# Kernel optimization log

Measured on AMD Instinct MI355X. Metric: run time of the kernel, lower is better.

Reference implementation:

```python
import jax, jax.numpy as jnp
import numpy as np
from jax import lax

B, L, D_MODEL = 2, 1024, 768
N_LAYER, D_STATE, D_CONV, EXPAND = 8, 16, 4, 2
D_INNER = EXPAND * D_MODEL          # 1536
DT_RANK = -(-D_MODEL // 16)         # 48 (MambaConfig 'auto')


def setup_inputs() -> dict:
    key = jax.random.key(0)
    ks = jax.random.split(key, 10)
    s = 0.02
    batch = jax.random.normal(ks[0], (B, D_MODEL, L), jnp.float32)
    lengths = jax.random.randint(ks[1], (B,), L // 2, L + 1)
    mask = jnp.arange(L)[None, :] < lengths[:, None]          # valid-prefix mask [B,L]
    norm_w = jnp.ones((N_LAYER, D_MODEL), jnp.float32)
    W_in = jax.random.normal(ks[2], (N_LAYER, 2 * D_INNER, D_MODEL), jnp.float32) * s
    conv_w = jax.random.normal(ks[3], (N_LAYER, D_INNER, D_CONV), jnp.float32) * 0.5
    conv_b = jnp.zeros((N_LAYER, D_INNER), jnp.float32)
    W_x = jax.random.normal(ks[4], (N_LAYER, DT_RANK + 2 * D_STATE, D_INNER), jnp.float32) * s
    W_dt = jax.random.normal(ks[5], (N_LAYER, D_INNER, DT_RANK), jnp.float32) * (DT_RANK ** -0.5)
    # mamba dt init: dt ~ logU[1e-3, 0.1], bias = softplus^-1(dt)
    dt = jnp.exp(jax.random.uniform(ks[6], (N_LAYER, D_INNER)) * (np.log(0.1) - np.log(1e-3)) + np.log(1e-3))
    b_dt = jnp.log(jnp.expm1(dt)).astype(jnp.float32)
    A_log = jnp.log(jnp.broadcast_to(jnp.arange(1, D_STATE + 1, dtype=jnp.float32), (N_LAYER, D_INNER, D_STATE))).copy()
    D_skip = jnp.ones((N_LAYER, D_INNER), jnp.float32)
    W_out = jax.random.normal(ks[7], (N_LAYER, D_MODEL, D_INNER), jnp.float32) * s
    normf_w = jnp.ones((D_MODEL,), jnp.float32)
    return dict(batch=batch, mask=mask, norm_w=norm_w, W_in=W_in, conv_w=conv_w, conv_b=conv_b,
                W_x=W_x, W_dt=W_dt, b_dt=b_dt, A_log=A_log, D_skip=D_skip, W_out=W_out, normf_w=normf_w)


def _rmsnorm(x, w, eps=1e-5):
    return x * w * lax.rsqrt(jnp.mean(x * x, axis=-1, keepdims=True) + eps)


def _mamba(x, W_in, cw, cb, W_x, W_dt, b_dt, A_log, Dsk, W_out):
    Bb, Ls, _ = x.shape
    d_inner, d_conv = cw.shape
    d_state = A_log.shape[-1]
    dt_rank = W_dt.shape[-1]
    xz = jnp.einsum('bld,ed->ble', x, W_in)                    # [B,L,2*d_inner]
    xc, z = jnp.split(xz, 2, axis=-1)
    # causal depthwise conv1d (+bias) then SiLU
    xt = lax.conv_general_dilated(xc.transpose(0, 2, 1), cw[:, None, :], (1,),
                                  [(d_conv - 1, 0)], feature_group_count=d_inner)
    u = jax.nn.silu(xt + cb[None, :, None]).transpose(0, 2, 1)  # [B,L,d_inner]
    dbl = jnp.einsum('bld,ed->ble', u, W_x)
    dtp, Bm, Cm = jnp.split(dbl, [dt_rank, dt_rank + d_state], axis=-1)
    delta = jax.nn.softplus(jnp.einsum('blr,dr->bld', dtp, W_dt) + b_dt)  # [B,L,d_inner]
    A = -jnp.exp(A_log)                                         # [d_inner,d_state]

    def step(h, t):
        d_t, b_t, c_t, u_t = t                                  # [B,di],[B,ds],[B,ds],[B,di]
        h = jnp.exp(d_t[..., None] * A) * h + (d_t * u_t)[..., None] * b_t[:, None, :]
        return h, jnp.einsum('bds,bs->bd', h, c_t)

    h0 = jnp.zeros((Bb, d_inner, d_state), x.dtype)
    _, ys = lax.scan(step, h0, (delta.transpose(1, 0, 2), Bm.transpose(1, 0, 2),
                                Cm.transpose(1, 0, 2), u.transpose(1, 0, 2)))
    y = ys.transpose(1, 0, 2) + u * Dsk
    return jnp.einsum('bld,ed->ble', y * jax.nn.silu(z), W_out)


def _forward(batch, mask, norm_w, W_in, conv_w, conv_b, W_x, W_dt, b_dt, A_log, D_skip, W_out, normf_w):
    h = jnp.transpose(batch, (0, 2, 1))                         # [B,L,D]
    for i in range(norm_w.shape[0]):                            # pre-norm residual blocks
        h = h + _mamba(_rmsnorm(h, norm_w[i]), W_in[i], conv_w[i], conv_b[i],
                       W_x[i], W_dt[i], b_dt[i], A_log[i], D_skip[i], W_out[i])
    h = _rmsnorm(h, normf_w)
    # last valid token: first False of mask (or L if none), minus 1
    inv = ~mask
    lengths = jnp.where(jnp.any(inv, axis=1), jnp.argmax(inv, axis=1), mask.shape[1]) - 1
    return jnp.take_along_axis(h, lengths[:, None, None], axis=1)[:, 0, :]


def reference(batch, mask, norm_w, W_in, conv_w, conv_b, W_x, W_dt, b_dt, A_log, D_skip, W_out, normf_w):
    return _forward(batch, mask, norm_w, W_in, conv_w, conv_b, W_x, W_dt, b_dt, A_log, D_skip, W_out, normf_w)
```

## Files before the change

kernel.cpp:

```cpp
#include <hip/hip_runtime.h>
#include <hip/hip_bf16.h>
#include <math.h>

#define BB 2
#define LL 1024
#define DM 768
#define NL 8
#define DS 16
#define DC 4
#define DI 1536
#define DTR 48
#define NTOK (BB*LL)
#define WXROWS (DTR + 2*DS)
#define NC 64
#define CT (LL/NC)
#define SKS 8
#define SKC (DI/SKS)
#define SK4 3
#define SK4C (DI/SK4)
#define DTB 8

typedef __attribute__((ext_vector_type(8))) short bf16x8;
typedef __attribute__((ext_vector_type(4))) float f32x4;

__device__ inline void gload_lds16(const void* g, void* l) {
    __builtin_amdgcn_global_load_lds(
        (const __attribute__((address_space(1))) unsigned int*)g,
        (__attribute__((address_space(3))) unsigned int*)l, 16, 0, 0);
}

__device__ inline int xcd_swz(int orig, int nwg) {
    return (orig & 7) * (nwg >> 3) + (orig >> 3);
}

__device__ inline void gemm_core64(
    const __hip_bfloat16* __restrict__ gA0,
    const __hip_bfloat16* __restrict__ gW0, const __hip_bfloat16* __restrict__ gW1,
    int kbeg, int kend, int w, int wr, int wc, int fr, int khi,
    f32x4 (&acc)[2][4])
{
    __shared__ short As[2048];
    __shared__ short Ws[4096];
    short* AsW = As + w * 512;
    short* WsW = Ws + w * 512;
    for (int k0 = kbeg; k0 < kend; k0 += 32) {
        gload_lds16(gA0 + k0, AsW);
        gload_lds16(gW0 + k0, WsW);
        gload_lds16(gW1 + k0, WsW + 2048);
        asm volatile("s_waitcnt vmcnt(0)" ::: "memory");
        __syncthreads();
        bf16x8 a4[2], b4[4];
        #pragma unroll
        for (int mi = 0; mi < 2; ++mi)
            a4[mi] = *(const bf16x8*)&As[(wr*32 + mi*16 + fr)*32 + khi*8];
        #pragma unroll
        for (int ni = 0; ni < 4; ++ni)
            b4[ni] = *(const bf16x8*)&Ws[(wc*64 + ni*16 + fr)*32 + khi*8];
        #pragma unroll
        for (int mi = 0; mi < 2; ++mi)
            #pragma unroll
            for (int ni = 0; ni < 4; ++ni)
                acc[mi][ni] = __builtin_amdgcn_mfma_f32_16x16x32_bf16(
                    a4[mi], b4[ni], acc[mi][ni], 0, 0, 0);
        __syncthreads();
    }
}

__global__ __launch_bounds__(256) void transpose_in_kernel(
    const float* __restrict__ batch, float* __restrict__ h)
{
    __shared__ float tile[32][33];
    const int b  = blockIdx.z;
    const int l0 = blockIdx.x * 32;
    const int d0 = blockIdx.y * 32;
    const int tx = threadIdx.x & 31;
    const int ty = threadIdx.x >> 5;
    #pragma unroll
    for (int i = ty; i < 32; i += 8)
        tile[i][tx] = batch[((size_t)b*DM + d0 + i)*LL + l0 + tx];
    __syncthreads();
    #pragma unroll
    for (int i = ty; i < 32; i += 8)
        h[((size_t)b*LL + l0 + i)*DM + d0 + tx] = tile[tx][i];
}

__global__ void lengths_kernel(const void* __restrict__ mask, int* __restrict__ lengths)
{
    int b = threadIdx.x;
    if (b >= BB) return;
    const unsigned int* mi = (const unsigned int*)mask;
    bool packed = (mi[0] == 0x01010101u);
    int cnt = 0;
    if (packed) {
        const unsigned char* mb = (const unsigned char*)mask;
        for (int i = 0; i < LL; ++i) cnt += (mb[(size_t)b*LL + i] != 0);
    } else {
        for (int i = 0; i < LL; ++i) cnt += (mi[(size_t)b*LL + i] != 0);
    }
    lengths[b] = cnt;
}

__global__ __launch_bounds__(256) void cvt_bf16_kernel(
    const float* __restrict__ in, __hip_bfloat16* __restrict__ o, int n)
{
    int i = (blockIdx.x * 256 + threadIdx.x) * 4;
    if (i >= n) return;
    float4 v = *(const float4*)(in + i);
    __hip_bfloat16 h0 = __float2bfloat16(v.x);
    __hip_bfloat16 h1 = __float2bfloat16(v.y);
    __hip_bfloat16 h2 = __float2bfloat16(v.z);
    __hip_bfloat16 h3 = __float2bfloat16(v.w);
    ushort4 r;
    r.x = *(unsigned short*)&h0; r.y = *(unsigned short*)&h1;
    r.z = *(unsigned short*)&h2; r.w = *(unsigned short*)&h3;
    *(ushort4*)(o + i) = r;
}

__global__ __launch_bounds__(256) void cvt_padrow_kernel(
    const float* __restrict__ in, __hip_bfloat16* __restrict__ o,
    int nrin, int nrout, int ncol, int nmat)
{
    int i = (blockIdx.x * 256 + threadIdx.x) * 4;
    int tot = nmat * nrout * ncol;
    if (i >= tot) return;
    int m = i / (nrout * ncol);
    int rem = i - m * (nrout * ncol);
    int r = rem / ncol;
    int c = rem - r * ncol;
    ushort4 rr = {0,0,0,0};
    if (r < nrin) {
        float4 v = *(const float4*)(in + ((size_t)m*nrin + r)*ncol + c);
        __hip_bfloat16 h0 = __float2bfloat16(v.x);
        __hip_bfloat16 h1 = __float2bfloat16(v.y);
        __hip_bfloat16 h2 = __float2bfloat16(v.z);
        __hip_bfloat16 h3 = __float2bfloat16(v.w);
        rr.x = *(unsigned short*)&h0; rr.y = *(unsigned short*)&h1;
        rr.z = *(unsigned short*)&h2; rr.w = *(unsigned short*)&h3;
    }
    *(ushort4*)(o + i) = rr;
}

__global__ __launch_bounds__(256) void rmsnorm_kernel(
    const float* __restrict__ x, const float* __restrict__ w,
    __hip_bfloat16* __restrict__ o)
{
    int tok = blockIdx.x;
    const float* xr = x + (size_t)tok * DM;
    float ss = 0.f;
    for (int j = threadIdx.x; j < DM; j += 256) { float v = xr[j]; ss += v*v; }
    #pragma unroll
    for (int off = 32; off > 0; off >>= 1) ss += __shfl_down(ss, off);
    __shared__ float red[4];
    int lane = threadIdx.x & 63, wv = threadIdx.x >> 6;
    if (lane == 0) red[wv] = ss;
    __syncthreads();
    if (threadIdx.x == 0) {
        float t = red[0] + red[1] + red[2] + red[3];
        red[0] = rsqrtf(t / (float)DM + 1e-5f);
    }
    __syncthreads();
    float r = red[0];
    for (int j = threadIdx.x; j < DM; j += 256)
        o[(size_t)tok*DM + j] = __float2bfloat16(xr[j] * w[j] * r);
}

__global__ __launch_bounds__(256) void gemm_mfma_kernel(
    const __hip_bfloat16* __restrict__ A,
    const __hip_bfloat16* __restrict__ W,
    __hip_bfloat16* __restrict__ C,
    int NT, int M, int N, int K)
{
    const int swz = xcd_swz(blockIdx.x, gridDim.x);
    const int bn = (swz % NT) * 128;
    const int bm = (swz / NT) * 64;
    const int t = threadIdx.x;
    const int w = t >> 6;
    const int lane = t & 63;
    const int wr = w >> 1, wc = w & 1;
    const int fr = lane & 15;
    const int khi = lane >> 4;

    f32x4 acc[2][4];
    #pragma unroll
    for (int mi = 0; mi < 2; ++mi)
        #pragma unroll
        for (int ni = 0; ni < 4; ++ni)
            acc[mi][ni] = (f32x4){0.f, 0.f, 0.f, 0.f};

    const int rowL = t >> 2;
    const int ks = (t & 3) * 8;
    gemm_core64(A + (size_t)(bm + rowL) * K + ks,
                W + (size_t)(bn + rowL) * K + ks,
                W + (size_t)(bn + 64 + rowL) * K + ks,
                0, K, w, wr, wc, fr, khi, acc);

    #pragma unroll
    for (int mi = 0; mi < 2; ++mi) {
        #pragma unroll
        for (int ni = 0; ni < 4; ++ni) {
            int gc = bn + wc*64 + ni*16 + fr;
            #pragma unroll
            for (int r = 0; r < 4; ++r) {
                int gr = bm + wr*32 + mi*16 + khi*4 + r;
                C[(size_t)gr * N + gc] = __float2bfloat16(acc[mi][ni][r]);
            }
        }
    }
}

__global__ __launch_bounds__(256) void gemm_mfma_splitk4(
    const __hip_bfloat16* __restrict__ A,
    const __hip_bfloat16* __restrict__ W,
    float* __restrict__ Cp)
{
    const int swz = xcd_swz(blockIdx.x, gridDim.x);
    const int bm = (swz / 18) * 64;
    const int r18 = swz % 18;
    const int bn = (r18 % 6) * 128;
    const int split = r18 / 6;
    const int t = threadIdx.x;
    const int w = t >> 6;
    const int lane = t & 63;
    const int wr = w >> 1, wc = w & 1;
    const int fr = lane & 15;
    const int khi = lane >> 4;

    f32x4 acc[2][4];
    #pragma unroll
    for (int mi = 0; mi < 2; ++mi)
        #pragma unroll
        for (int ni = 0; ni < 4; ++ni)
            acc[mi][ni] = (f32x4){0.f, 0.f, 0.f, 0.f};

    const int rowL = t >> 2;
    const int ks = (t & 3) * 8;
    const int kbeg = split * SK4C;
    gemm_core64(A + (size_t)(bm + rowL) * DI + ks,
                W + (size_t)(bn + rowL) * DI + ks,
                W + (size_t)(bn + 64 + rowL) * DI + ks,
                kbeg, kbeg + SK4C, w, wr, wc, fr, khi, acc);

    #pragma unroll
    for (int mi = 0; mi < 2; ++mi) {
        #pragma unroll
        for (int ni = 0; ni < 4; ++ni) {
            int gc = bn + wc*64 + ni*16 + fr;
            #pragma unroll
            for (int r = 0; r < 4; ++r) {
                int gr = bm + wr*32 + mi*16 + khi*4 + r;
                Cp[((size_t)split*NTOK + gr)*DM + gc] = acc[mi][ni][r];
            }
        }
    }
}

__global__ __launch_bounds__(256) void reduce_add_norm_kernel(
    const float* __restrict__ Cp, float* __restrict__ h,
    const float* __restrict__ nw, __hip_bfloat16* __restrict__ xn)
{
    int tok = blockIdx.x;
    int tid = threadIdx.x;
    float v[3];
    float ss = 0.f;
    #pragma unroll
    for (int r = 0; r < 3; ++r) {
        int j = tid + r*256;
        size_t o = (size_t)tok*DM + j;
        float x = h[o] + Cp[o] + Cp[(size_t)NTOK*DM + o] + Cp[2*(size_t)NTOK*DM + o];
        h[o] = x;
        v[r] = x;
        ss += x*x;
    }
    if (!nw) return;
    #pragma unroll
    for (int off = 32; off > 0; off >>= 1) ss += __shfl_down(ss, off);
    __shared__ float red[4];
    int lane = tid & 63, wv = tid >> 6;
    if (lane == 0) red[wv] = ss;
    __syncthreads();
    if (tid == 0) {
        float t = red[0] + red[1] + red[2] + red[3];
        red[0] = rsqrtf(t / (float)DM + 1e-5f);
    }
    __syncthreads();
    float rinv = red[0];
    #pragma unroll
    for (int r = 0; r < 3; ++r) {
        int j = tid + r*256;
        xn[(size_t)tok*DM + j] = __float2bfloat16(v[r] * nw[j] * rinv);
    }
}

__global__ __launch_bounds__(256) void gemm_mfma_skinny(
    const __hip_bfloat16* __restrict__ A,
    const __hip_bfloat16* __restrict__ W,
    float* __restrict__ Cp)
{
    const int split = blockIdx.x;
    const int bm = blockIdx.y * 64;
    const int t = threadIdx.x;
    const int w = t >> 6;
    const int lane = t & 63;
    const int wr = w >> 1, wc = w & 1;
    const int fr = lane & 15;
    const int khi = lane >> 4;

    f32x4 acc[2][4];
    #pragma unroll
    for (int mi = 0; mi < 2; ++mi)
        #pragma unroll
        for (int ni = 0; ni < 4; ++ni)
            acc[mi][ni] = (f32x4){0.f, 0.f, 0.f, 0.f};

    const int rowL = t >> 2;
    const int ks = (t & 3) * 8;
    const int kbeg = split * SKC;
    gemm_core64(A + (size_t)(bm + rowL) * DI + ks,
                W + (size_t)rowL * DI + ks,
                W + (size_t)(64 + rowL) * DI + ks,
                kbeg, kbeg + SKC, w, wr, wc, fr, khi, acc);

    #pragma unroll
    for (int mi = 0; mi < 2; ++mi) {
        #pragma unroll
        for (int ni = 0; ni < 4; ++ni) {
            int gc = wc*64 + ni*16 + fr;
            if (gc >= WXROWS) continue;
            #pragma unroll
            for (int r = 0; r < 4; ++r) {
                int gr = bm + wr*32 + mi*16 + khi*4 + r;
                Cp[((size_t)split*NTOK + gr)*WXROWS + gc] = acc[mi][ni][r];
            }
        }
    }
}

__global__ __launch_bounds__(256) void reduce_delta_kernel(
    const float* __restrict__ Cp,
    const float* __restrict__ W_dt, const float* __restrict__ b_dt,
    float* __restrict__ dbl, __hip_bfloat16* __restrict__ delta)
{
    __shared__ float ld[DTB*DTR];
    const int tid = threadIdx.x;
    const int d = blockIdx.x * 256 + tid;
    const int t0 = blockIdx.y * DTB;
    for (int j = tid; j < DTB*DTR; j += 256) {
        int tt = j / DTR, jj = j - tt*DTR;
        float s = 0.f;
        #pragma unroll
        for (int p = 0; p < SKS; ++p)
            s += Cp[((size_t)p*NTOK + t0 + tt)*WXROWS + jj];
        ld[j] = s;
    }
    if (blockIdx.x == 0) {
        for (int j = tid; j < DTB*WXROWS; j += 256) {
            int tt = j / WXROWS, jj = j - tt*WXROWS;
            float s = 0.f;
            #pragma unroll
            for (int p = 0; p < SKS; ++p)
                s += Cp[((size_t)p*NTOK + t0 + tt)*WXROWS + jj];
            dbl[(size_t)(t0 + tt)*WXROWS + jj] = s;
        }
    }
    float wdt[DTR];
    #pragma unroll
    for (int j = 0; j < DTR; j += 4) {
        float4 v = *(const float4*)(W_dt + (size_t)d*DTR + j);
        wdt[j] = v.x; wdt[j+1] = v.y; wdt[j+2] = v.z; wdt[j+3] = v.w;
    }
    const float bdt = b_dt[d];
    __syncthreads();
    #pragma unroll
    for (int tt = 0; tt < DTB; ++tt) {
        float dt = bdt;
        #pragma unroll
        for (int j = 0; j < DTR; ++j) dt = fmaf(ld[tt*DTR + j], wdt[j], dt);
        dt = (dt > 20.f) ? dt : log1pf(__expf(dt));
        delta[(size_t)(t0 + tt)*DI + d] = __float2bfloat16(dt);
    }
}

__global__ __launch_bounds__(256) void conv_silu_kernel(
    const __hip_bfloat16* __restrict__ xz, const float* __restrict__ cw,
    const float* __restrict__ cb, __hip_bfloat16* __restrict__ u)
{
    int idx = blockIdx.x * 256 + threadIdx.x;
    if (idx >= NTOK*DI/8) return;
    const int dg  = idx % (DI/8);
    const int row = idx / (DI/8);
    const int l   = row % LL;
    const int d0  = dg * 8;

    float acc[8];
    {
        float4 c0 = *(const float4*)(cb + d0);
        float4 c1 = *(const float4*)(cb + d0 + 4);
        acc[0]=c0.x; acc[1]=c0.y; acc[2]=c0.z; acc[3]=c0.w;
        acc[4]=c1.x; acc[5]=c1.y; acc[6]=c1.z; acc[7]=c1.w;
    }
    float4 cwj[8];
    #pragma unroll
    for (int j = 0; j < 8; ++j)
        cwj[j] = *(const float4*)(cw + (size_t)(d0 + j)*4);

    #pragma unroll
    for (int k = 0; k < 4; ++k) {
        int ls = l - 3 + k;
        if (ls < 0) continue;
        bf16x8 v = *(const bf16x8*)(xz + (size_t)(row - 3 + k)*(2*DI) + d0);
        const __hip_bfloat16* vp = (const __hip_bfloat16*)&v;
        #pragma unroll
        for (int j = 0; j < 8; ++j) {
            float xv = __bfloat162float(vp[j]);
            float wv = (k == 0) ? cwj[j].x : (k == 1) ? cwj[j].y : (k == 2) ? cwj[j].z : cwj[j].w;
            acc[j] = fmaf(xv, wv, acc[j]);
        }
    }
    bf16x8 r;
    __hip_bfloat16* rp = (__hip_bfloat16*)&r;
    #pragma unroll
    for (int j = 0; j < 8; ++j) {
        float s = acc[j] / (1.f + __expf(-acc[j]));
        rp[j] = __float2bfloat16(s);
    }
    *(bf16x8*)(u + (size_t)row*DI + d0) = r;
}

__global__ __launch_bounds__(256) void scan_phaseA(
    const __hip_bfloat16* __restrict__ delta, const __hip_bfloat16* __restrict__ u,
    const float* __restrict__ dbl, const float* __restrict__ A_log,
    float* __restrict__ Psum, float* __restrict__ Hsum)
{
    const int d = blockIdx.x * 256 + threadIdx.x;
    const int c = blockIdx.y;
    const int b = blockIdx.z;
    float A[DS], P[DS], hl[DS];
    #pragma unroll
    for (int s = 0; s < DS; ++s) {
        A[s] = -expf(A_log[(size_t)d*DS + s]);
        P[s] = 1.f; hl[s] = 0.f;
    }
    const int t0 = c * CT;
    for (int t = t0; t < t0 + CT; ++t) {
        const size_t row = (size_t)b*LL + t;
        const float* bc = dbl + row*WXROWS + DTR;
        float dt = __bfloat162float(delta[row*DI + d]);
        float du = dt * __bfloat162float(u[row*DI + d]);
        #pragma unroll
        for (int s = 0; s < DS; ++s) {
            float a = __expf(dt * A[s]);
            P[s] *= a;
            hl[s] = fmaf(a, hl[s], du * bc[s]);
        }
    }
    const size_t off = (((size_t)b*NC + c)*DI + d)*DS;
    #pragma unroll
    for (int s = 0; s < DS; ++s) { Psum[off+s] = P[s]; Hsum[off+s] = hl[s]; }
}

__global__ __launch_bounds__(256) void scan_phaseB(
    const float* __restrict__ Psum, const float* __restrict__ Hsum,
    float* __restrict__ Hin)
{
    const int gid = blockIdx.x * 256 + threadIdx.x;
    if (gid >= BB*DI*DS) return;
    const int b = gid / (DI*DS);
    const int r = gid % (DI*DS);
    float hc = 0.f;
    for (int c = 0; c < NC; ++c) {
        const size_t off = ((size_t)(b*NC + c))*DI*DS + r;
        Hin[off] = hc;
        hc = fmaf(Psum[off], hc, Hsum[off]);
    }
}

__global__ __launch_bounds__(256) void scan_phaseC(
    const __hip_bfloat16* __restrict__ delta, const __hip_bfloat16* __restrict__ u,
    const float* __restrict__ dbl, const __hip_bfloat16* __restrict__ xz,
    const float* __restrict__ A_log, const float* __restrict__ Dsk,
    const float* __restrict__ Hin, __hip_bfloat16* __restrict__ yfull)
{
    const int d = blockIdx.x * 256 + threadIdx.x;
    const int c = blockIdx.y;
    const int b = blockIdx.z;
    float A[DS], h[DS];
    const size_t hoff = (((size_t)b*NC + c)*DI + d)*DS;
    #pragma unroll
    for (int s = 0; s < DS; ++s) {
        A[s] = -expf(A_log[(size_t)d*DS + s]);
        h[s] = Hin[hoff + s];
    }
    const float dsk = Dsk[d];
    const int t0 = c * CT;
    for (int t = t0; t < t0 + CT; ++t) {
        const size_t row = (size_t)b*LL + t;
        const float* bc = dbl + row*WXROWS + DTR;
        float dt = __bfloat162float(delta[row*DI + d]);
        float ut = __bfloat162float(u[row*DI + d]);
        float du = dt * ut;
        float y = 0.f;
        #pragma unroll
        for (int s = 0; s < DS; ++s) {
            float a = __expf(dt * A[s]);
            h[s] = fmaf(a, h[s], du * bc[s]);
            y = fmaf(h[s], bc[DS+s], y);
        }
        float zt = __bfloat162float(xz[row*(2*DI) + DI + d]);
        float sz = zt / (1.f + __expf(-zt));
        yfull[row*DI + d] = __float2bfloat16((y + ut * dsk) * sz);
    }
}

__global__ __launch_bounds__(256) void final_kernel(
    const float* __restrict__ h, const float* __restrict__ w,
    const int* __restrict__ lengths, float* __restrict__ out)
{
    int b = blockIdx.x;
    int idx = lengths[b] - 1;
    const float* xr = h + ((size_t)b*LL + idx)*DM;
    float ss = 0.f;
    for (int j = threadIdx.x; j < DM; j += 256) { float v = xr[j]; ss += v*v; }
    #pragma unroll
    for (int off = 32; off > 0; off >>= 1) ss += __shfl_down(ss, off);
    __shared__ float red[4];
    int lane = threadIdx.x & 63, wv = threadIdx.x >> 6;
    if (lane == 0) red[wv] = ss;
    __syncthreads();
    if (threadIdx.x == 0) {
        float t = red[0] + red[1] + red[2] + red[3];
        red[0] = rsqrtf(t / (float)DM + 1e-5f);
    }
    __syncthreads();
    float r = red[0];
    for (int j = threadIdx.x; j < DM; j += 256)
        out[(size_t)b*DM + j] = xr[j] * w[j] * r;
}

extern "C" void kernel_launch(void* const* d_in, const int* in_sizes, int n_in,
                              void* d_out, int out_size, void* d_ws, size_t ws_size,
                              hipStream_t stream)
{
    const float* batch   = (const float*)d_in[0];
    const void*  mask    = d_in[1];
    const float* norm_w  = (const float*)d_in[2];
    const float* W_in    = (const float*)d_in[3];
    const float* conv_w  = (const float*)d_in[4];
    const float* conv_b  = (const float*)d_in[5];
    const float* W_x     = (const float*)d_in[6];
    const float* W_dt    = (const float*)d_in[7];
    const float* b_dt    = (const float*)d_in[8];
    const float* A_log   = (const float*)d_in[9];
    const float* D_skip  = (const float*)d_in[10];
    const float* W_out   = (const float*)d_in[11];
    const float* normf_w = (const float*)d_in[12];
    float* out = (float*)d_out;

    float* ws   = (float*)d_ws;
    float* h    = ws;
    float* dbl  = h   + (size_t)NTOK*DM;
    float* scr  = dbl + (size_t)NTOK*WXROWS;
    const size_t SEG = (size_t)BB*NC*DI*DS;
    float* dblp = scr;
    float* Psum = scr;
    float* Hsum = scr + SEG;
    float* Hin  = scr + 2*SEG;
    float* Cp4  = scr;
    __hip_bfloat16* xz_bf    = (__hip_bfloat16*)(scr + 3*SEG);
    __hip_bfloat16* xn_bf    = xz_bf + (size_t)NTOK*2*DI;
    __hip_bfloat16* u_bf     = xn_bf + (size_t)NTOK*DM;
    __hip_bfloat16* delta_bf = u_bf  + (size_t)NTOK*DI;
    __hip_bfloat16* y_bf     = delta_bf + (size_t)NTOK*DI;
    __hip_bfloat16* wbase    = y_bf + (size_t)NTOK*DI;

    const size_t WIN_L  = (size_t)2*DI*DM;
    const size_t WOUT_L = (size_t)DM*DI;
    const size_t WXP_L  = (size_t)128*DI;
    const size_t WSUM   = WIN_L + WOUT_L + WXP_L;

    size_t need_all = (size_t)((char*)(wbase + (size_t)NL*WSUM) - (char*)d_ws) + 256;
    const bool all = ws_size >= need_all;
    const int nlw = all ? NL : 1;

    __hip_bfloat16* Win_b  = wbase;
    __hip_bfloat16* Wout_b = Win_b  + (size_t)nlw*WIN_L;
    __hip_bfloat16* Wxp_b  = Wout_b + (size_t)nlw*WOUT_L;
    int* lengths = (int*)(Wxp_b + (size_t)nlw*WXP_L);

    transpose_in_kernel<<<dim3(LL/32, DM/32, BB), 256, 0, stream>>>(batch, h);
    lengths_kernel<<<1, 64, 0, stream>>>(mask, lengths);

    if (all) {
        cvt_bf16_kernel<<<(int)(NL*WIN_L/4/256), 256, 0, stream>>>(W_in, Win_b, (int)(NL*WIN_L));
        cvt_bf16_kernel<<<(int)(NL*WOUT_L/4/256), 256, 0, stream>>>(W_out, Wout_b, (int)(NL*WOUT_L));
        cvt_padrow_kernel<<<(int)(NL*WXP_L/4/256), 256, 0, stream>>>(
            W_x, Wxp_b, WXROWS, 128, DI, NL);
    }

    rmsnorm_kernel<<<NTOK, 256, 0, stream>>>(h, norm_w, xn_bf);

    for (int i = 0; i < NL; ++i) {
        const float* cwi  = conv_w + (size_t)i * DI * DC;
        const float* cbi  = conv_b + (size_t)i * DI;
        const float* Wdti = W_dt  + (size_t)i * DI * DTR;
        const float* bdti = b_dt  + (size_t)i * DI;
        const float* Ali  = A_log + (size_t)i * DI * DS;
        const float* Dski = D_skip + (size_t)i * DI;

        if (!all) {
            cvt_bf16_kernel<<<(int)(WIN_L/4/256), 256, 0, stream>>>(
                W_in + (size_t)i*WIN_L, Win_b, (int)WIN_L);
            cvt_bf16_kernel<<<(int)(WOUT_L/4/256), 256, 0, stream>>>(
                W_out + (size_t)i*WOUT_L, Wout_b, (int)WOUT_L);
            cvt_padrow_kernel<<<(int)(WXP_L/4/256), 256, 0, stream>>>(
                W_x + (size_t)i*WXROWS*DI, Wxp_b, WXROWS, 128, DI, 1);
        }
        const __hip_bfloat16* Win_l  = Win_b  + (all ? (size_t)i*WIN_L  : 0);
        const __hip_bfloat16* Wout_l = Wout_b + (all ? (size_t)i*WOUT_L : 0);
        const __hip_bfloat16* Wxp_l  = Wxp_b  + (all ? (size_t)i*WXP_L  : 0);

        gemm_mfma_kernel<<<(2*DI/128)*(NTOK/64), 256, 0, stream>>>(
            xn_bf, Win_l, xz_bf, 2*DI/128, NTOK, 2*DI, DM);
        conv_silu_kernel<<<(NTOK*DI/8 + 255)/256, 256, 0, stream>>>(xz_bf, cwi, cbi, u_bf);
        gemm_mfma_skinny<<<dim3(SKS, NTOK/64), 256, 0, stream>>>(u_bf, Wxp_l, dblp);
        reduce_delta_kernel<<<dim3(DI/256, NTOK/DTB), 256, 0, stream>>>(
            dblp, Wdti, bdti, dbl, delta_bf);
        scan_phaseA<<<dim3(DI/256, NC, BB), 256, 0, stream>>>(
            delta_bf, u_bf, dbl, Ali, Psum, Hsum);
        scan_phaseB<<<(BB*DI*DS + 255)/256, 256, 0, stream>>>(Psum, Hsum, Hin);
        scan_phaseC<<<dim3(DI/256, NC, BB), 256, 0, stream>>>(
            delta_bf, u_bf, dbl, xz_bf, Ali, Dski, Hin, y_bf);
        gemm_mfma_splitk4<<<SK4*(NTOK/64)*(DM/128), 256, 0, stream>>>(
            y_bf, Wout_l, Cp4);
        reduce_add_norm_kernel<<<NTOK, 256, 0, stream>>>(
            Cp4, h, (i < NL-1) ? (norm_w + (size_t)(i+1)*DM) : nullptr, xn_bf);
    }

    final_kernel<<<BB, 256, 0, stream>>>(h, normf_w, lengths, out);
}
```

Measured before the change: 1.121 ms.

## Double-buffer LDS tiles in bf16 GEMM core to overlap loads with MFMA

The shared GEMM core now keeps two LDS buffers for the A and W tiles. It preloads the first K-slice, then, while running MFMAs on the current slice, issues the async global-to-LDS loads for the next one. The goal is to hide global-load latency behind compute and drop one barrier per iteration. In exchange it doubles LDS use per block, which may lower occupancy. There is also no explicit vmcnt wait before the prefetched buffer is read, so correctness depends on the compiler inserting that wait.

```diff
diff --git a/kernel.cpp b/kernel.cpp
--- a/kernel.cpp
+++ b/kernel.cpp
@@ -39,23 +39,35 @@
     int kbeg, int kend, int w, int wr, int wc, int fr, int khi,
     f32x4 (&acc)[2][4])
 {
-    __shared__ short As[2048];
-    __shared__ short Ws[4096];
-    short* AsW = As + w * 512;
-    short* WsW = Ws + w * 512;
+    __shared__ short As[2][2048];
+    __shared__ short Ws[2][4096];
+    {
+        short* a = &As[0][w*512];
+        short* b = &Ws[0][w*512];
+        gload_lds16(gA0 + kbeg, a);
+        gload_lds16(gW0 + kbeg, b);
+        gload_lds16(gW1 + kbeg, b + 2048);
+    }
+    asm volatile("s_waitcnt vmcnt(0)" ::: "memory");
+    __syncthreads();
+    int cur = 0;
     for (int k0 = kbeg; k0 < kend; k0 += 32) {
-        gload_lds16(gA0 + k0, AsW);
-        gload_lds16(gW0 + k0, WsW);
-        gload_lds16(gW1 + k0, WsW + 2048);
-        asm volatile("s_waitcnt vmcnt(0)" ::: "memory");
-        __syncthreads();
+        if (k0 + 32 < kend) {
+            short* a = &As[cur^1][w*512];
+            short* b = &Ws[cur^1][w*512];
+            gload_lds16(gA0 + k0 + 32, a);
+            gload_lds16(gW0 + k0 + 32, b);
+            gload_lds16(gW1 + k0 + 32, b + 2048);
+        }
+        const short* Ab = &As[cur][0];
+        const short* Wb = &Ws[cur][0];
         bf16x8 a4[2], b4[4];
         #pragma unroll
         for (int mi = 0; mi < 2; ++mi)
-            a4[mi] = *(const bf16x8*)&As[(wr*32 + mi*16 + fr)*32 + khi*8];
+            a4[mi] = *(const bf16x8*)&Ab[(wr*32 + mi*16 + fr)*32 + khi*8];
         #pragma unroll
         for (int ni = 0; ni < 4; ++ni)
-            b4[ni] = *(const bf16x8*)&Ws[(wc*64 + ni*16 + fr)*32 + khi*8];
+            b4[ni] = *(const bf16x8*)&Wb[(wc*64 + ni*16 + fr)*32 + khi*8];
         #pragma unroll
         for (int mi = 0; mi < 2; ++mi)
             #pragma unroll
@@ -63,6 +75,7 @@
                 acc[mi][ni] = __builtin_amdgcn_mfma_f32_16x16x32_bf16(
                     a4[mi], b4[ni], acc[mi][ni], 0, 0, 0);
         __syncthreads();
+        cur ^= 1;
     }
 }
 
```

New measurement: 1.138 ms. About the same (+1.6%).
